# Optimization experiments

Hardware: AMD Instinct MI355X
Metric: run time of the kernel (lower is better)

Reference implementation:

```python
import jax, jax.numpy as jnp
import numpy as np

N = 20000      # nodes in both graphs
B = 128        # graphs in batch
E = 320000     # edges (avg degree 16)
F_IN = 768     # num_features (bert/graph feature dim)
RAW_F = 5000   # raw feature dim (hardcoded 5000 in source)
H = 256        # nhid
C = 4          # num_classes


def _gcn(x, src, dst, W, b):
    # PyG GCNConv: add self loops, symmetric D^-1/2 (A+I) D^-1/2 normalization
    n = x.shape[0]
    h = x @ W
    loop = jnp.arange(n, dtype=src.dtype)
    s = jnp.concatenate([src, loop])
    d = jnp.concatenate([dst, loop])
    deg = jax.ops.segment_sum(jnp.ones_like(d, dtype=h.dtype), d, num_segments=n)
    dinv = jax.lax.rsqrt(jnp.maximum(deg, 1.0))
    norm = (dinv[s] * dinv[d])[:, None]
    out = jax.ops.segment_sum(h[s] * norm, d, num_segments=n)
    return out + b


def _segment_mean(x, seg, num_segments):
    s = jax.ops.segment_sum(x, seg, num_segments=num_segments)
    cnt = jax.ops.segment_sum(jnp.ones((x.shape[0],), x.dtype), seg, num_segments=num_segments)
    return s / jnp.maximum(cnt, 1.0)[:, None]


def _prelu(x, a):
    return jnp.where(x >= 0, x, a * x)


def setup_inputs():
    key = jax.random.key(0)
    k = jax.random.split(key, 16)
    graph_x = jax.random.normal(k[0], (N, F_IN), jnp.float32)
    bert_x = jax.random.normal(k[1], (N, F_IN), jnp.float32)
    data_x = jax.random.normal(k[2], (N, RAW_F), jnp.float32) * 0.05
    edge_index = jax.random.randint(k[3], (2, E), 0, N, jnp.int32)
    raw_edge_index = jax.random.randint(k[4], (2, E), 0, N, jnp.int32)
    batch = ((jnp.arange(N) * B) // N).astype(jnp.int32)  # sorted, covers all B graphs
    rootindex = jax.random.randint(k[5], (B,), 0, N, jnp.int32)

    def lin(kk, fin, fout):
        return jax.random.normal(kk, (fin, fout), jnp.float32) * (1.0 / np.sqrt(fin))

    W1 = lin(k[6], F_IN, H); b1 = jnp.zeros((H,), jnp.float32)
    Wc0 = lin(k[7], RAW_F, H); bc0 = jnp.zeros((H,), jnp.float32)
    Wc1 = lin(k[8], H, H); bc1 = jnp.zeros((H,), jnp.float32)
    Wc2 = lin(k[9], H, H); bc2 = jnp.zeros((H,), jnp.float32)
    Wl1 = lin(k[10], 2 * RAW_F, 2 * H); bl1 = jnp.zeros((2 * H,), jnp.float32)
    Wl2 = lin(k[11], 2 * H, H); bl2 = jnp.zeros((H,), jnp.float32)
    W5 = lin(k[12], 5 * H, C); b5 = jnp.zeros((C,), jnp.float32)
    prelu_a = jnp.asarray(0.25, jnp.float32)
    return dict(graph_x=graph_x, bert_x=bert_x, data_x=data_x,
                edge_index=edge_index, raw_edge_index=raw_edge_index,
                graph_batch=batch, x_batch=batch, rootindex=rootindex,
                W1=W1, b1=b1, Wc0=Wc0, bc0=bc0, Wc1=Wc1, bc1=bc1, Wc2=Wc2, bc2=bc2,
                Wl1=Wl1, bl1=bl1, Wl2=Wl2, bl2=bl2, prelu_a=prelu_a, W5=W5, b5=b5)


def reference(graph_x, bert_x, data_x, edge_index, raw_edge_index, graph_batch,
              x_batch, rootindex, W1, b1, Wc0, bc0, Wc1, bc1, Wc2, bc2,
              Wl1, bl1, Wl2, bl2, prelu_a, W5, b5):
    # branch 1: GCNConv over graph_x (bert_user=0), relu, global max pool
    x = jax.nn.relu(_gcn(graph_x, edge_index[0], edge_index[1], W1, b1))
    x = jax.ops.segment_max(x, graph_batch, num_segments=B)   # [B, H]
    # branch 2: scatter_mean of raw features + root node, MLP w/ PReLU (eval: dropout = id)
    new_x = _segment_mean(data_x, x_batch, B)                 # [B, RAW_F]
    root = data_x[rootindex]                                  # [B, RAW_F]
    new_x = jnp.concatenate([new_x, root], axis=1)            # [B, 2*RAW_F]
    new_x = _prelu(new_x @ Wl1 + bl1, prelu_a)
    new_x = _prelu(new_x @ Wl2 + bl2, prelu_a)                # [B, H]
    # branch 3 (boost=1): 3 GCN layers over raw graph, mean pool each layer
    x_one = data_x
    pools = []
    for (W, b) in ((Wc0, bc0), (Wc1, bc1), (Wc2, bc2)):
        x_one = jax.nn.relu(_gcn(x_one, raw_edge_index[0], raw_edge_index[1], W, b))
        pools.append(_segment_mean(x_one, x_batch, B))
    out = jnp.concatenate(pools + [new_x, x], axis=1)         # [B, 5*H]
    return jax.nn.log_softmax(out @ W5 + b5, axis=1)
```

## Files before the change

kernel.cpp:

```cpp
#include <hip/hip_runtime.h>
#include <math.h>

#define NN   20000
#define BG   128
#define EE   320000
#define FIN  768
#define RAWF 5000
#define KP   5120
#define CATK 10240
#define HD   256
#define NC   4

typedef __attribute__((ext_vector_type(4))) float          f32x4;
typedef __attribute__((ext_vector_type(8))) unsigned short u16x8;
typedef __attribute__((ext_vector_type(4))) unsigned short u16x4;
typedef __attribute__((ext_vector_type(8))) __bf16         bf16x8;

__device__ __forceinline__ unsigned short f2bf(float f) {
  unsigned u = __float_as_uint(f);
  u += 0x7FFFu + ((u >> 16) & 1u);
  return (unsigned short)(u >> 16);
}
__device__ __forceinline__ float bf2f(unsigned short u) {
  return __uint_as_float((unsigned)u << 16);
}

static inline int ceil_div(int a, int b) { return (a + b - 1) / b; }

__global__ void count_deg2_k(const int* __restrict__ ei, const int* __restrict__ rei,
                             int* __restrict__ deg1, int* __restrict__ deg2) {
  int i = blockIdx.x * 256 + threadIdx.x;
  if (i < EE) atomicAdd(&deg1[ei[EE + i]], 1);
  else if (i < 2 * EE) atomicAdd(&deg2[rei[i]], 1);
}

__global__ __launch_bounds__(1024) void scan_local_k(const int* __restrict__ deg1,
                                                     const int* __restrict__ deg2,
                                                     int* __restrict__ excl,
                                                     int* __restrict__ bsum, int nb) {
  const int* deg = blockIdx.y ? deg2 : deg1;
  int* ex = excl + (size_t)blockIdx.y * NN;
  int* bs = bsum + (size_t)blockIdx.y * nb;
  __shared__ int wsum[16];
  int t = threadIdx.x, lane = t & 63, w = t >> 6;
  int i = blockIdx.x * 1024 + t;
  int v = (i < NN) ? deg[i] : 0;
  int acc = v;
#pragma unroll
  for (int off = 1; off < 64; off <<= 1) {
    int o = __shfl_up(acc, off, 64);
    if (lane >= off) acc += o;
  }
  if (lane == 63) wsum[w] = acc;
  __syncthreads();
  if (w == 0 && lane < 16) {
    int s = wsum[lane];
#pragma unroll
    for (int off = 1; off < 16; off <<= 1) {
      int o = __shfl_up(s, off, 64);
      if (lane >= off) s += o;
    }
    wsum[lane] = s;
  }
  __syncthreads();
  if (w > 0) acc += wsum[w - 1];
  if (i < NN) ex[i] = acc - v;
  if (t == 1023) bs[blockIdx.x] = acc;
}

__global__ void scan_tops_k(const int* __restrict__ bsum, int* __restrict__ boff,
                            int* __restrict__ end1, int* __restrict__ end2, int nb) {
  if (threadIdx.x == 0) {
    int run = 0;
    for (int b = 0; b < nb; ++b) { boff[b] = run; run += bsum[b]; }
    *end1 = run;
    run = 0;
    for (int b = 0; b < nb; ++b) { boff[nb + b] = run; run += bsum[nb + b]; }
    *end2 = run;
  }
}

__global__ __launch_bounds__(1024) void scan_add_k(
    const int* __restrict__ excl, const int* __restrict__ boff,
    const int* __restrict__ deg1, const int* __restrict__ deg2,
    int* __restrict__ rp1, int* __restrict__ rp2,
    int* __restrict__ cur1, int* __restrict__ cur2,
    float* __restrict__ dv1, float* __restrict__ dv2, int nb) {
  int y = blockIdx.y;
  const int* deg = y ? deg2 : deg1;
  int* rp = y ? rp2 : rp1;
  int* cur = y ? cur2 : cur1;
  float* dv = y ? dv2 : dv1;
  int i = blockIdx.x * 1024 + threadIdx.x;
  if (i < NN) {
    int v = excl[(size_t)y * NN + i] + boff[y * nb + blockIdx.x];
    rp[i] = v;
    cur[i] = v;
    dv[i] = rsqrtf((float)(deg[i] + 1));
  }
}

__global__ void scatter_k(const int* __restrict__ ei, const int* __restrict__ rei,
                          int* __restrict__ cur1, int* __restrict__ cur2,
                          int* __restrict__ col1, int* __restrict__ col2) {
  int i = blockIdx.x * 256 + threadIdx.x;
  int y = blockIdx.y;
  if (i < EE) {
    const int* e = y ? rei : ei;
    int* cur = y ? cur2 : cur1;
    int* col = y ? col2 : col1;
    int d = e[EE + i];
    int p = atomicAdd(&cur[d], 1);
    col[p] = e[i];
  }
}

__global__ void segbounds_k(const int* __restrict__ batch, int* __restrict__ s,
                            int* __restrict__ e, int n) {
  int i = blockIdx.x * 256 + threadIdx.x;
  if (i >= n) return;
  int b = batch[i];
  if (i == 0 || batch[i - 1] != b) s[b] = i;
  if (i == n - 1 || batch[i + 1] != b) e[b] = i + 1;
}

__global__ __launch_bounds__(256) void trans_k(
    const float* __restrict__ i0, unsigned short* __restrict__ o0,
    const float* __restrict__ i1, unsigned short* __restrict__ o1,
    const float* __restrict__ i2, unsigned short* __restrict__ o2,
    const float* __restrict__ i3, unsigned short* __restrict__ o3,
    const float* __restrict__ i4, unsigned short* __restrict__ o4) {
  __shared__ unsigned short tile[32][34];
  int b = blockIdx.x;
  const float* in; unsigned short* out;
  int K, N, Kout, tx, lid;
  if (b < 192)        { in=i0; out=o0; K=768;   N=256; Kout=768;   tx=24;  lid=b; }
  else if (b < 1472)  { in=i1; out=o1; K=5000;  N=256; Kout=5120;  tx=160; lid=b-192; }
  else if (b < 1536)  { in=i2; out=o2; K=256;   N=256; Kout=256;   tx=8;   lid=b-1472; }
  else if (b < 1600)  { in=i3; out=o3; K=256;   N=256; Kout=256;   tx=8;   lid=b-1536; }
  else                { in=i4; out=o4; K=10000; N=512; Kout=10240; tx=320; lid=b-1600; }
  int k0 = (lid % tx) * 32, n0 = (lid / tx) * 32;
  int txx = threadIdx.x & 31, tyy = threadIdx.x >> 5;
#pragma unroll
  for (int r = 0; r < 32; r += 8) {
    int k = k0 + tyy + r, n = n0 + txx;
    float v = (k < K) ? in[(size_t)k * N + n] : 0.f;
    tile[tyy + r][txx] = f2bf(v);
  }
  __syncthreads();
#pragma unroll
  for (int r = 0; r < 32; r += 8) {
    int n = n0 + tyy + r, k = k0 + txx;
    out[(size_t)n * Kout + k] = tile[txx][tyy + r];
  }
}

__global__ void conv_graphx_k(const float* __restrict__ in, unsigned short* __restrict__ out) {
  size_t i = (size_t)(blockIdx.x * 256 + threadIdx.x) * 8;
  f32x4 a = *(const f32x4*)(in + i);
  f32x4 b = *(const f32x4*)(in + i + 4);
  u16x8 o;
  o[0]=f2bf(a[0]); o[1]=f2bf(a[1]); o[2]=f2bf(a[2]); o[3]=f2bf(a[3]);
  o[4]=f2bf(b[0]); o[5]=f2bf(b[1]); o[6]=f2bf(b[2]); o[7]=f2bf(b[3]);
  *(u16x8*)(out + i) = o;
}

__global__ __launch_bounds__(256) void conv_pool_k(const float* __restrict__ x,
                                                   unsigned short* __restrict__ xb,
                                                   unsigned short* __restrict__ cat,
                                                   const int* __restrict__ segs,
                                                   const int* __restrict__ sege) {
  int g = blockIdx.x;
  int c = blockIdx.y * 256 + threadIdx.x;
  int s = segs[g], e = sege[g];
  bool vc = c < RAWF;
  float sum = 0.f;
  if (xb) {
    int i = s;
    for (; i + 2 <= e; i += 2) {
      float v0 = 0.f, v1 = 0.f;
      if (vc) { v0 = x[(size_t)i * RAWF + c]; v1 = x[(size_t)(i + 1) * RAWF + c]; }
      xb[(size_t)i * KP + c] = f2bf(v0);
      xb[(size_t)(i + 1) * KP + c] = f2bf(v1);
      sum += v0 + v1;
    }
    for (; i < e; ++i) {
      float v = 0.f;
      if (vc) v = x[(size_t)i * RAWF + c];
      xb[(size_t)i * KP + c] = f2bf(v);
      sum += v;
    }
  } else if (vc) {
    float a0 = 0, a1 = 0, a2 = 0, a3 = 0;
    int i = s;
    for (; i + 4 <= e; i += 4) {
      a0 += x[(size_t)(i + 0) * RAWF + c];
      a1 += x[(size_t)(i + 1) * RAWF + c];
      a2 += x[(size_t)(i + 2) * RAWF + c];
      a3 += x[(size_t)(i + 3) * RAWF + c];
    }
    for (; i < e; ++i) a0 += x[(size_t)i * RAWF + c];
    sum = (a0 + a1) + (a2 + a3);
  }
  if (vc) cat[(size_t)g * CATK + c] = f2bf(sum / (float)(e - s));
}

__global__ void root_cat_k(const float* __restrict__ data_x, const int* __restrict__ root,
                           unsigned short* __restrict__ cat) {
  int g = blockIdx.x;
  int c = blockIdx.y * 256 + threadIdx.x;
  if (c >= CATK - RAWF) return;
  unsigned short v = 0;
  if (c < RAWF) v = f2bf(data_x[(size_t)root[g] * RAWF + c]);
  cat[(size_t)g * CATK + RAWF + c] = v;
}

template <bool ABF16>
__global__ __launch_bounds__(256) void gemm_k(
    const void* __restrict__ Av, int Astride,
    const unsigned short* __restrict__ Bt, int Bstride,
    float* __restrict__ C, int M, int N, int Kreal, int kchunk, int atomic_out) {
  __shared__ unsigned short As[128 * 40];
  __shared__ unsigned short Bs[128 * 40];
  const int tid = threadIdx.x;
  const int lane = tid & 63, wave = tid >> 6;
  const int quad = lane >> 4, l16 = lane & 15;
  const int koff = quad * 8;
  const int bn = blockIdx.x * 128, bm = blockIdx.y * 128;
  const int wm = (wave >> 1) * 64, wn = (wave & 1) * 64;
  const int kbegin = blockIdx.z * kchunk;
  int kend = kbegin + kchunk; if (kend > Kreal) kend = Kreal;

  const int brow = tid >> 2, bcol = (tid & 3) * 8;
  const int arow_f = tid >> 3, acol_f = (tid & 7) * 4;

  u16x8 pb[2];
  u16x8 pa_b[2];
  f32x4 pa_f[4];

  auto load_tile = [&](int k0) {
#pragma unroll
    for (int i = 0; i < 2; ++i) {
      int gk = k0 + bcol;
      bool ok = ABF16 ? true : (gk + 8 <= kend);
      u16x8 v = (u16x8)(unsigned short)0;
      if (ok) v = *(const u16x8*)(Bt + (size_t)(bn + i * 64 + brow) * Bstride + gk);
      pb[i] = v;
    }
    if (ABF16) {
      const unsigned short* A = (const unsigned short*)Av;
#pragma unroll
      for (int i = 0; i < 2; ++i) {
        int r = bm + i * 64 + brow;
        u16x8 v = (u16x8)(unsigned short)0;
        if (r < M) v = *(const u16x8*)(A + (size_t)r * Astride + k0 + bcol);
        pa_b[i] = v;
      }
    } else {
      const float* A = (const float*)Av;
#pragma unroll
      for (int i = 0; i < 4; ++i) {
        int r = bm + i * 32 + arow_f;
        int gk = k0 + acol_f;
        f32x4 v = (f32x4)0.f;
        if (r < M && gk + 4 <= kend) v = *(const f32x4*)(A + (size_t)r * Astride + gk);
        pa_f[i] = v;
      }
    }
  };
  auto store_tile = [&]() {
#pragma unroll
    for (int i = 0; i < 2; ++i)
      *(u16x8*)&Bs[(i * 64 + brow) * 40 + bcol] = pb[i];
    if (ABF16) {
#pragma unroll
      for (int i = 0; i < 2; ++i)
        *(u16x8*)&As[(i * 64 + brow) * 40 + bcol] = pa_b[i];
    } else {
#pragma unroll
      for (int i = 0; i < 4; ++i) {
        u16x4 h;
        h[0] = f2bf(pa_f[i][0]); h[1] = f2bf(pa_f[i][1]);
        h[2] = f2bf(pa_f[i][2]); h[3] = f2bf(pa_f[i][3]);
        *(u16x4*)&As[(i * 32 + arow_f) * 40 + acol_f] = h;
      }
    }
  };

  f32x4 acc[4][4] = {};
  load_tile(kbegin);
  for (int k0 = kbegin; k0 < kend; k0 += 32) {
    store_tile();
    __syncthreads();
    int k1 = k0 + 32;
    if (k1 < kend) load_tile(k1);
    u16x8 ar[4], br[4];
#pragma unroll
    for (int i = 0; i < 4; ++i) ar[i] = *(const u16x8*)&As[(wm + i * 16 + l16) * 40 + koff];
#pragma unroll
    for (int j = 0; j < 4; ++j) br[j] = *(const u16x8*)&Bs[(wn + j * 16 + l16) * 40 + koff];
#pragma unroll
    for (int i = 0; i < 4; ++i)
#pragma unroll
      for (int j = 0; j < 4; ++j)
        acc[i][j] = __builtin_amdgcn_mfma_f32_16x16x32_bf16(
            __builtin_bit_cast(bf16x8, ar[i]), __builtin_bit_cast(bf16x8, br[j]),
            acc[i][j], 0, 0, 0);
    __syncthreads();
  }
#pragma unroll
  for (int i = 0; i < 4; ++i)
#pragma unroll
    for (int rr = 0; rr < 4; ++rr) {
      int grow = bm + wm + i * 16 + quad * 4 + rr;
      if (grow >= M) continue;
#pragma unroll
      for (int j = 0; j < 4; ++j) {
        int gcol = bn + wn + j * 16 + l16;
        if (gcol >= N) continue;
        float v = acc[i][j][rr];
        if (atomic_out) atomicAdd(&C[(size_t)grow * N + gcol], v);
        else C[(size_t)grow * N + gcol] = v;
      }
    }
}

__global__ __launch_bounds__(256) void gcn_agg_k(
    const float* __restrict__ h, const int* __restrict__ rowptr,
    const int* __restrict__ col, const float* __restrict__ dinv,
    const float* __restrict__ bias, unsigned short* __restrict__ outb, int n) {
  int wave = threadIdx.x >> 6, lane = threadIdx.x & 63;
  int node = blockIdx.x * 4 + wave;
  if (node >= n) return;
  int f = lane * 4;
  float di = dinv[node];
  f32x4 acc = *(const f32x4*)(h + (size_t)node * HD + f) * di;
  int beg = rowptr[node], end = rowptr[node + 1];
  int e = beg;
  for (; e + 4 <= end; e += 4) {
    int s0 = col[e], s1 = col[e + 1], s2 = col[e + 2], s3 = col[e + 3];
    float w0 = dinv[s0], w1 = dinv[s1], w2 = dinv[s2], w3 = dinv[s3];
    f32x4 h0 = *(const f32x4*)(h + (size_t)s0 * HD + f);
    f32x4 h1 = *(const f32x4*)(h + (size_t)s1 * HD + f);
    f32x4 h2 = *(const f32x4*)(h + (size_t)s2 * HD + f);
    f32x4 h3 = *(const f32x4*)(h + (size_t)s3 * HD + f);
    acc += h0 * w0; acc += h1 * w1; acc += h2 * w2; acc += h3 * w3;
  }
  for (; e < end; ++e) {
    int s = col[e];
    acc += *(const f32x4*)(h + (size_t)s * HD + f) * dinv[s];
  }
  f32x4 b = *(const f32x4*)(bias + f);
  acc = acc * di + b;
  u16x4 o;
#pragma unroll
  for (int q = 0; q < 4; ++q) o[q] = f2bf(fmaxf(acc[q], 0.f));
  *(u16x4*)(outb + (size_t)node * HD + f) = o;
}

__global__ __launch_bounds__(256) void seg_pool_bf16_k(const unsigned short* __restrict__ src,
                                                       const int* __restrict__ segs,
                                                       const int* __restrict__ sege,
                                                       float* __restrict__ dst, int dstride,
                                                       int doff, int mode) {
  int g = blockIdx.x, f = threadIdx.x;
  int s = segs[g], e = sege[g];
  float a0, a1, a2, a3;
  if (mode == 1) { a0 = a1 = a2 = a3 = -INFINITY; } else { a0 = a1 = a2 = a3 = 0.f; }
  int i = s;
  for (; i + 4 <= e; i += 4) {
    float v0 = bf2f(src[(size_t)(i + 0) * HD + f]);
    float v1 = bf2f(src[(size_t)(i + 1) * HD + f]);
    float v2 = bf2f(src[(size_t)(i + 2) * HD + f]);
    float v3 = bf2f(src[(size_t)(i + 3) * HD + f]);
    if (mode == 1) { a0 = fmaxf(a0, v0); a1 = fmaxf(a1, v1); a2 = fmaxf(a2, v2); a3 = fmaxf(a3, v3); }
    else           { a0 += v0; a1 += v1; a2 += v2; a3 += v3; }
  }
  for (; i < e; ++i) {
    float v = bf2f(src[(size_t)i * HD + f]);
    if (mode == 1) a0 = fmaxf(a0, v); else a0 += v;
  }
  float acc;
  if (mode == 1) acc = fmaxf(fmaxf(a0, a1), fmaxf(a2, a3));
  else {
    acc = (a0 + a1) + (a2 + a3);
    acc /= (float)((e - s) > 0 ? (e - s) : 1);
  }
  dst[(size_t)g * dstride + doff + f] = acc;
}

__global__ void bias_prelu_k(const float* __restrict__ in, const float* __restrict__ bias,
                             const float* __restrict__ pa, float* __restrict__ out,
                             int total, int cols) {
  int i = blockIdx.x * 256 + threadIdx.x;
  if (i >= total) return;
  float v = in[i] + bias[i % cols];
  float a = *pa;
  out[i] = (v >= 0.f) ? v : a * v;
}

__global__ __launch_bounds__(256) void gemm_e_k(const float* __restrict__ t1,
                                                const float* __restrict__ Wl2,
                                                const float* __restrict__ bl2,
                                                const float* __restrict__ pa,
                                                float* __restrict__ pools) {
  int b = blockIdx.x, n = threadIdx.x;
  float acc = 0.f;
  for (int k = 0; k < 512; ++k) acc = fmaf(t1[b * 512 + k], Wl2[k * 256 + n], acc);
  acc += bl2[n];
  float a = *pa;
  acc = (acc >= 0.f) ? acc : a * acc;
  pools[(size_t)b * 1280 + 768 + n] = acc;
}

__global__ __launch_bounds__(256) void final_k(const float* __restrict__ pools,
                                               const float* __restrict__ W5,
                                               const float* __restrict__ b5,
                                               float* __restrict__ out) {
  __shared__ float red[256][4];
  int b = blockIdx.x, t = threadIdx.x;
  float a0 = 0, a1 = 0, a2 = 0, a3 = 0;
  for (int i = t; i < 1280; i += 256) {
    float p = pools[(size_t)b * 1280 + i];
    a0 = fmaf(p, W5[i * 4 + 0], a0);
    a1 = fmaf(p, W5[i * 4 + 1], a1);
    a2 = fmaf(p, W5[i * 4 + 2], a2);
    a3 = fmaf(p, W5[i * 4 + 3], a3);
  }
  red[t][0] = a0; red[t][1] = a1; red[t][2] = a2; red[t][3] = a3;
  __syncthreads();
  for (int off = 128; off >= 1; off >>= 1) {
    if (t < off)
      for (int c = 0; c < 4; ++c) red[t][c] += red[t + off][c];
    __syncthreads();
  }
  if (t == 0) {
    float z[4];
    for (int c = 0; c < 4; ++c) z[c] = red[0][c] + b5[c];
    float m = fmaxf(fmaxf(z[0], z[1]), fmaxf(z[2], z[3]));
    float s = 0.f;
    for (int c = 0; c < 4; ++c) s += expf(z[c] - m);
    float lse = logf(s);
    for (int c = 0; c < 4; ++c) out[b * 4 + c] = z[c] - m - lse;
  }
}

extern "C" void kernel_launch(void* const* d_in, const int* in_sizes, int n_in,
                              void* d_out, int out_size, void* d_ws, size_t ws_size,
                              hipStream_t stream) {
  const float* graph_x = (const float*)d_in[0];
  const float* data_x  = (const float*)d_in[2];
  const int*   ei      = (const int*)d_in[3];
  const int*   rei     = (const int*)d_in[4];
  const int*   batch   = (const int*)d_in[5];
  const int*   rooti   = (const int*)d_in[7];
  const float* W1  = (const float*)d_in[8];   const float* b1  = (const float*)d_in[9];
  const float* Wc0 = (const float*)d_in[10];  const float* bc0 = (const float*)d_in[11];
  const float* Wc1 = (const float*)d_in[12];  const float* bc1 = (const float*)d_in[13];
  const float* Wc2 = (const float*)d_in[14];  const float* bc2 = (const float*)d_in[15];
  const float* Wl1 = (const float*)d_in[16];  const float* bl1 = (const float*)d_in[17];
  const float* Wl2 = (const float*)d_in[18];  const float* bl2 = (const float*)d_in[19];
  const float* pa  = (const float*)d_in[20];
  const float* W5  = (const float*)d_in[21];  const float* b5  = (const float*)d_in[22];
  float* out = (float*)d_out;

  char* ws = (char*)d_ws;
  size_t off = 0;
  auto take = [&](size_t bytes) -> void* {
    void* p = ws + off;
    off += (bytes + 255) & ~(size_t)255;
    return p;
  };
  const int NB = ceil_div(NN, 1024);

  int *deg1, *deg2, *rp1, *rp2, *cur1, *cur2, *col1, *col2, *excl, *bsum, *boff, *segs, *sege;
  float *dv1, *dv2, *hA, *Cd, *t1, *pools;
  unsigned short *W1t, *Wc0t, *Wc1t, *Wc2t, *Wl1t, *gxb, *catb, *hBb, *Axb;

  auto alloc_all = [&](bool withAxb) {
    off = 0;
    deg1 = (int*)take(NN * 4);   deg2 = (int*)take(NN * 4);
    rp1  = (int*)take((NN + 1) * 4); rp2 = (int*)take((NN + 1) * 4);
    cur1 = (int*)take(NN * 4);   cur2 = (int*)take(NN * 4);
    col1 = (int*)take(EE * 4);   col2 = (int*)take(EE * 4);
    dv1  = (float*)take(NN * 4); dv2  = (float*)take(NN * 4);
    excl = (int*)take((size_t)2 * NN * 4);
    bsum = (int*)take(2 * NB * 4); boff = (int*)take(2 * NB * 4);
    segs = (int*)take(BG * 4);   sege = (int*)take(BG * 4);
    W1t  = (unsigned short*)take((size_t)HD * FIN * 2);
    Wc0t = (unsigned short*)take((size_t)HD * KP * 2);
    Wc1t = (unsigned short*)take((size_t)HD * HD * 2);
    Wc2t = (unsigned short*)take((size_t)HD * HD * 2);
    Wl1t = (unsigned short*)take((size_t)512 * CATK * 2);
    gxb  = (unsigned short*)take((size_t)NN * FIN * 2);
    catb = (unsigned short*)take((size_t)BG * CATK * 2);
    Axb  = withAxb ? (unsigned short*)take((size_t)NN * KP * 2) : nullptr;
    hA   = (float*)take((size_t)NN * HD * 4);
    hBb  = (unsigned short*)take((size_t)NN * HD * 2);
    Cd   = (float*)take((size_t)BG * 512 * 4);
    t1   = (float*)take((size_t)BG * 512 * 4);
    pools = (float*)take((size_t)BG * 1280 * 4);
  };
  alloc_all(true);
  if (off > ws_size) alloc_all(false);
  const bool pathA = (Axb != nullptr);

  hipMemsetAsync(deg1, 0, (size_t)2 * ((NN * 4 + 255) & ~255), stream);
  hipMemsetAsync(Cd, 0, (size_t)BG * 512 * 4, stream);

  count_deg2_k<<<ceil_div(2 * EE, 256), 256, 0, stream>>>(ei, rei, deg1, deg2);
  scan_local_k<<<dim3(NB, 2), 1024, 0, stream>>>(deg1, deg2, excl, bsum, NB);
  scan_tops_k<<<1, 64, 0, stream>>>(bsum, boff, rp1 + NN, rp2 + NN, NB);
  scan_add_k<<<dim3(NB, 2), 1024, 0, stream>>>(excl, boff, deg1, deg2, rp1, rp2,
                                               cur1, cur2, dv1, dv2, NB);
  scatter_k<<<dim3(ceil_div(EE, 256), 2), 256, 0, stream>>>(ei, rei, cur1, cur2, col1, col2);
  segbounds_k<<<ceil_div(NN, 256), 256, 0, stream>>>(batch, segs, sege, NN);

  trans_k<<<6720, 256, 0, stream>>>(W1, W1t, Wc0, Wc0t, Wc1, Wc1t, Wc2, Wc2t, Wl1, Wl1t);

  conv_graphx_k<<<(NN * FIN) / (256 * 8), 256, 0, stream>>>(graph_x, gxb);
  conv_pool_k<<<dim3(BG, KP / 256), 256, 0, stream>>>(data_x, Axb, catb, segs, sege);
  root_cat_k<<<dim3(BG, ceil_div(CATK - RAWF, 256)), 256, 0, stream>>>(data_x, rooti, catb);

  int mt = ceil_div(NN, 128);

  hipMemsetAsync(hA, 0, (size_t)NN * HD * 4, stream);
  gemm_k<true><<<dim3(2, mt, 3), 256, 0, stream>>>(gxb, FIN, W1t, FIN, hA, NN, HD, FIN, 256, 1);
  gcn_agg_k<<<ceil_div(NN, 4), 256, 0, stream>>>(hA, rp1, col1, dv1, b1, hBb, NN);
  seg_pool_bf16_k<<<BG, 256, 0, stream>>>(hBb, segs, sege, pools, 1280, 1024, 1);

  hipMemsetAsync(hA, 0, (size_t)NN * HD * 4, stream);
  if (pathA)
    gemm_k<true><<<dim3(2, mt, 4), 256, 0, stream>>>(Axb, KP, Wc0t, KP, hA, NN, HD, KP, 1280, 1);
  else
    gemm_k<false><<<dim3(2, mt, 4), 256, 0, stream>>>(data_x, RAWF, Wc0t, KP, hA, NN, HD, RAWF, 1256, 1);
  gcn_agg_k<<<ceil_div(NN, 4), 256, 0, stream>>>(hA, rp2, col2, dv2, bc0, hBb, NN);
  seg_pool_bf16_k<<<BG, 256, 0, stream>>>(hBb, segs, sege, pools, 1280, 0, 0);

  hipMemsetAsync(hA, 0, (size_t)NN * HD * 4, stream);
  gemm_k<true><<<dim3(2, mt, 2), 256, 0, stream>>>(hBb, HD, Wc1t, HD, hA, NN, HD, HD, 128, 1);
  gcn_agg_k<<<ceil_div(NN, 4), 256, 0, stream>>>(hA, rp2, col2, dv2, bc1, hBb, NN);
  seg_pool_bf16_k<<<BG, 256, 0, stream>>>(hBb, segs, sege, pools, 1280, 256, 0);

  hipMemsetAsync(hA, 0, (size_t)NN * HD * 4, stream);
  gemm_k<true><<<dim3(2, mt, 2), 256, 0, stream>>>(hBb, HD, Wc2t, HD, hA, NN, HD, HD, 128, 1);
  gcn_agg_k<<<ceil_div(NN, 4), 256, 0, stream>>>(hA, rp2, col2, dv2, bc2, hBb, NN);
  seg_pool_bf16_k<<<BG, 256, 0, stream>>>(hBb, segs, sege, pools, 1280, 512, 0);

  gemm_k<true><<<dim3(4, 1, 32), 256, 0, stream>>>(catb, CATK, Wl1t, CATK, Cd, BG, 512, CATK, 320, 1);
  bias_prelu_k<<<ceil_div(BG * 512, 256), 256, 0, stream>>>(Cd, bl1, pa, t1, BG * 512, 512);
  gemm_e_k<<<BG, 256, 0, stream>>>(t1, Wl2, bl2, pa, pools);

  final_k<<<BG, 256, 0, stream>>>(pools, W5, b5, out);
}
```

Measured before the change: 1.369 ms.

## Fuse conversions, prescale GEMM rows by dinv, swizzle tiles, parallelize scan tops

Several independent changes land together. The graph_x bf16 conversion pass is removed so the first GEMM reads fp32 directly, and root gathering is merged into the vectorised pooling kernel. The source-side dinv is applied in the GEMM epilogue so the aggregation only sums neighbour rows, and bias+PReLU is folded into the second MLP kernel. It also adds a grouped tile remap for the 2-column GEMMs, changes split-K factors, and replaces the serial top-level scan with a warp scan. Together these drop launches and intermediate buffers, at the cost of fp32 A-tile loads in the first GEMM and less split-K parallelism.

```diff
diff --git a/kernel.cpp b/kernel.cpp
--- a/kernel.cpp
+++ b/kernel.cpp
@@ -70,13 +70,18 @@
 
 __global__ void scan_tops_k(const int* __restrict__ bsum, int* __restrict__ boff,
                             int* __restrict__ end1, int* __restrict__ end2, int nb) {
-  if (threadIdx.x == 0) {
-    int run = 0;
-    for (int b = 0; b < nb; ++b) { boff[b] = run; run += bsum[b]; }
-    *end1 = run;
-    run = 0;
-    for (int b = 0; b < nb; ++b) { boff[nb + b] = run; run += bsum[nb + b]; }
-    *end2 = run;
+  int t = threadIdx.x;
+  int half = t >> 5, idx = t & 31;
+  int v = (idx < nb) ? bsum[half * nb + idx] : 0;
+  int acc = v;
+#pragma unroll
+  for (int off = 1; off < 32; off <<= 1) {
+    int o = __shfl_up(acc, off, 32);
+    if (idx >= off) acc += o;
+  }
+  if (idx < nb) boff[half * nb + idx] = acc - v;
+  if (idx == nb - 1) {
+    if (half == 0) *end1 = acc; else *end2 = acc;
   }
 }
 
@@ -155,78 +160,75 @@
   }
 }
 
-__global__ void conv_graphx_k(const float* __restrict__ in, unsigned short* __restrict__ out) {
-  size_t i = (size_t)(blockIdx.x * 256 + threadIdx.x) * 8;
-  f32x4 a = *(const f32x4*)(in + i);
-  f32x4 b = *(const f32x4*)(in + i + 4);
-  u16x8 o;
-  o[0]=f2bf(a[0]); o[1]=f2bf(a[1]); o[2]=f2bf(a[2]); o[3]=f2bf(a[3]);
-  o[4]=f2bf(b[0]); o[5]=f2bf(b[1]); o[6]=f2bf(b[2]); o[7]=f2bf(b[3]);
-  *(u16x8*)(out + i) = o;
-}
-
 __global__ __launch_bounds__(256) void conv_pool_k(const float* __restrict__ x,
                                                    unsigned short* __restrict__ xb,
                                                    unsigned short* __restrict__ cat,
                                                    const int* __restrict__ segs,
-                                                   const int* __restrict__ sege) {
+                                                   const int* __restrict__ sege,
+                                                   const int* __restrict__ root) {
   int g = blockIdx.x;
-  int c = blockIdx.y * 256 + threadIdx.x;
+  if (blockIdx.y >= KP / 256) {
+    int c = (blockIdx.y - KP / 256) * 256 + threadIdx.x;
+    if (c < CATK - RAWF) {
+      unsigned short v = 0;
+      if (c < RAWF) v = f2bf(x[(size_t)root[g] * RAWF + c]);
+      cat[(size_t)g * CATK + RAWF + c] = v;
+    }
+    return;
+  }
+  __shared__ f32x4 part[4][64];
+  int wave = threadIdx.x >> 6, lane = threadIdx.x & 63;
+  int c = blockIdx.y * 256 + lane * 4;
   int s = segs[g], e = sege[g];
-  bool vc = c < RAWF;
-  float sum = 0.f;
-  if (xb) {
-    int i = s;
-    for (; i + 2 <= e; i += 2) {
-      float v0 = 0.f, v1 = 0.f;
-      if (vc) { v0 = x[(size_t)i * RAWF + c]; v1 = x[(size_t)(i + 1) * RAWF + c]; }
-      xb[(size_t)i * KP + c] = f2bf(v0);
-      xb[(size_t)(i + 1) * KP + c] = f2bf(v1);
-      sum += v0 + v1;
-    }
-    for (; i < e; ++i) {
-      float v = 0.f;
-      if (vc) v = x[(size_t)i * RAWF + c];
-      xb[(size_t)i * KP + c] = f2bf(v);
-      sum += v;
-    }
-  } else if (vc) {
-    float a0 = 0, a1 = 0, a2 = 0, a3 = 0;
-    int i = s;
-    for (; i + 4 <= e; i += 4) {
-      a0 += x[(size_t)(i + 0) * RAWF + c];
-      a1 += x[(size_t)(i + 1) * RAWF + c];
-      a2 += x[(size_t)(i + 2) * RAWF + c];
-      a3 += x[(size_t)(i + 3) * RAWF + c];
-    }
-    for (; i < e; ++i) a0 += x[(size_t)i * RAWF + c];
-    sum = (a0 + a1) + (a2 + a3);
-  }
-  if (vc) cat[(size_t)g * CATK + c] = f2bf(sum / (float)(e - s));
-}
-
-__global__ void root_cat_k(const float* __restrict__ data_x, const int* __restrict__ root,
-                           unsigned short* __restrict__ cat) {
-  int g = blockIdx.x;
-  int c = blockIdx.y * 256 + threadIdx.x;
-  if (c >= CATK - RAWF) return;
-  unsigned short v = 0;
-  if (c < RAWF) v = f2bf(data_x[(size_t)root[g] * RAWF + c]);
-  cat[(size_t)g * CATK + RAWF + c] = v;
+  bool v4 = (c + 4 <= RAWF);
+  f32x4 sum = (f32x4)0.f;
+  for (int i = s + wave; i < e; i += 4) {
+    f32x4 v = (f32x4)0.f;
+    if (v4) v = *(const f32x4*)(x + (size_t)i * RAWF + c);
+    if (xb) {
+      u16x4 h;
+      h[0] = f2bf(v[0]); h[1] = f2bf(v[1]); h[2] = f2bf(v[2]); h[3] = f2bf(v[3]);
+      *(u16x4*)(xb + (size_t)i * KP + c) = h;
+    }
+    sum += v;
+  }
+  part[wave][lane] = sum;
+  __syncthreads();
+  if (threadIdx.x < 64 && v4) {
+    f32x4 tot = part[0][lane] + part[1][lane] + part[2][lane] + part[3][lane];
+    float cnt = (float)(e - s);
+    u16x4 o;
+    o[0] = f2bf(tot[0] / cnt); o[1] = f2bf(tot[1] / cnt);
+    o[2] = f2bf(tot[2] / cnt); o[3] = f2bf(tot[3] / cnt);
+    *(u16x4*)(cat + (size_t)g * CATK + c) = o;
+  }
 }
 
 template <bool ABF16>
 __global__ __launch_bounds__(256) void gemm_k(
     const void* __restrict__ Av, int Astride,
     const unsigned short* __restrict__ Bt, int Bstride,
-    float* __restrict__ C, int M, int N, int Kreal, int kchunk, int atomic_out) {
+    float* __restrict__ C, const float* __restrict__ escale,
+    int M, int N, int Kreal, int kchunk, int atomic_out) {
   __shared__ unsigned short As[128 * 40];
   __shared__ unsigned short Bs[128 * 40];
   const int tid = threadIdx.x;
   const int lane = tid & 63, wave = tid >> 6;
   const int quad = lane >> 4, l16 = lane & 15;
   const int koff = quad * 8;
-  const int bn = blockIdx.x * 128, bm = blockIdx.y * 128;
+
+  int xt = blockIdx.x, yt = blockIdx.y;
+  if (gridDim.x == 2) {
+    const int MT = gridDim.y;
+    int flat = (yt << 1) | xt;
+    int gp = flat >> 4;
+    int ybase = gp << 3;
+    int rem = MT - ybase;
+    int j = flat & 15;
+    if (rem >= 8) { xt = j >> 3; yt = ybase + (j & 7); }
+    else          { xt = (j >= rem); yt = ybase + (xt ? j - rem : j); }
+  }
+  const int bn = xt * 128, bm = yt * 128;
   const int wm = (wave >> 1) * 64, wn = (wave & 1) * 64;
   const int kbegin = blockIdx.z * kchunk;
   int kend = kbegin + kchunk; if (kend > Kreal) kend = Kreal;
@@ -314,11 +316,12 @@
     for (int rr = 0; rr < 4; ++rr) {
       int grow = bm + wm + i * 16 + quad * 4 + rr;
       if (grow >= M) continue;
+      float sc = escale ? escale[grow] : 1.f;
 #pragma unroll
       for (int j = 0; j < 4; ++j) {
         int gcol = bn + wn + j * 16 + l16;
         if (gcol >= N) continue;
-        float v = acc[i][j][rr];
+        float v = acc[i][j][rr] * sc;
         if (atomic_out) atomicAdd(&C[(size_t)grow * N + gcol], v);
         else C[(size_t)grow * N + gcol] = v;
       }
@@ -333,23 +336,20 @@
   int node = blockIdx.x * 4 + wave;
   if (node >= n) return;
   int f = lane * 4;
-  float di = dinv[node];
-  f32x4 acc = *(const f32x4*)(h + (size_t)node * HD + f) * di;
+  f32x4 acc = *(const f32x4*)(h + (size_t)node * HD + f);
   int beg = rowptr[node], end = rowptr[node + 1];
   int e = beg;
   for (; e + 4 <= end; e += 4) {
     int s0 = col[e], s1 = col[e + 1], s2 = col[e + 2], s3 = col[e + 3];
-    float w0 = dinv[s0], w1 = dinv[s1], w2 = dinv[s2], w3 = dinv[s3];
     f32x4 h0 = *(const f32x4*)(h + (size_t)s0 * HD + f);
     f32x4 h1 = *(const f32x4*)(h + (size_t)s1 * HD + f);
     f32x4 h2 = *(const f32x4*)(h + (size_t)s2 * HD + f);
     f32x4 h3 = *(const f32x4*)(h + (size_t)s3 * HD + f);
-    acc += h0 * w0; acc += h1 * w1; acc += h2 * w2; acc += h3 * w3;
-  }
-  for (; e < end; ++e) {
-    int s = col[e];
-    acc += *(const f32x4*)(h + (size_t)s * HD + f) * dinv[s];
-  }
+    acc += h0; acc += h1; acc += h2; acc += h3;
+  }
+  for (; e < end; ++e)
+    acc += *(const f32x4*)(h + (size_t)col[e] * HD + f);
+  float di = dinv[node];
   f32x4 b = *(const f32x4*)(bias + f);
   acc = acc * di + b;
   u16x4 o;
@@ -389,26 +389,23 @@
   dst[(size_t)g * dstride + doff + f] = acc;
 }
 
-__global__ void bias_prelu_k(const float* __restrict__ in, const float* __restrict__ bias,
-                             const float* __restrict__ pa, float* __restrict__ out,
-                             int total, int cols) {
-  int i = blockIdx.x * 256 + threadIdx.x;
-  if (i >= total) return;
-  float v = in[i] + bias[i % cols];
-  float a = *pa;
-  out[i] = (v >= 0.f) ? v : a * v;
-}
-
-__global__ __launch_bounds__(256) void gemm_e_k(const float* __restrict__ t1,
+__global__ __launch_bounds__(256) void gemm_e_k(const float* __restrict__ Cd,
+                                                const float* __restrict__ bl1,
                                                 const float* __restrict__ Wl2,
                                                 const float* __restrict__ bl2,
                                                 const float* __restrict__ pa,
                                                 float* __restrict__ pools) {
+  __shared__ float t[512];
   int b = blockIdx.x, n = threadIdx.x;
+  float a = *pa;
+  for (int k = n; k < 512; k += 256) {
+    float v = Cd[(size_t)b * 512 + k] + bl1[k];
+    t[k] = (v >= 0.f) ? v : a * v;
+  }
+  __syncthreads();
   float acc = 0.f;
-  for (int k = 0; k < 512; ++k) acc = fmaf(t1[b * 512 + k], Wl2[k * 256 + n], acc);
+  for (int k = 0; k < 512; ++k) acc = fmaf(t[k], Wl2[k * 256 + n], acc);
   acc += bl2[n];
-  float a = *pa;
   acc = (acc >= 0.f) ? acc : a * acc;
   pools[(size_t)b * 1280 + 768 + n] = acc;
 }
@@ -474,8 +471,8 @@
   const int NB = ceil_div(NN, 1024);
 
   int *deg1, *deg2, *rp1, *rp2, *cur1, *cur2, *col1, *col2, *excl, *bsum, *boff, *segs, *sege;
-  float *dv1, *dv2, *hA, *Cd, *t1, *pools;
-  unsigned short *W1t, *Wc0t, *Wc1t, *Wc2t, *Wl1t, *gxb, *catb, *hBb, *Axb;
+  float *dv1, *dv2, *hA, *Cd, *pools;
+  unsigned short *W1t, *Wc0t, *Wc1t, *Wc2t, *Wl1t, *catb, *hBb, *Axb;
 
   auto alloc_all = [&](bool withAxb) {
     off = 0;
@@ -492,13 +489,11 @@
     Wc1t = (unsigned short*)take((size_t)HD * HD * 2);
     Wc2t = (unsigned short*)take((size_t)HD * HD * 2);
     Wl1t = (unsigned short*)take((size_t)512 * CATK * 2);
-    gxb  = (unsigned short*)take((size_t)NN * FIN * 2);
     catb = (unsigned short*)take((size_t)BG * CATK * 2);
     Axb  = withAxb ? (unsigned short*)take((size_t)NN * KP * 2) : nullptr;
     hA   = (float*)take((size_t)NN * HD * 4);
     hBb  = (unsigned short*)take((size_t)NN * HD * 2);
     Cd   = (float*)take((size_t)BG * 512 * 4);
-    t1   = (float*)take((size_t)BG * 512 * 4);
     pools = (float*)take((size_t)BG * 1280 * 4);
   };
   alloc_all(true);
@@ -518,38 +513,42 @@
 
   trans_k<<<6720, 256, 0, stream>>>(W1, W1t, Wc0, Wc0t, Wc1, Wc1t, Wc2, Wc2t, Wl1, Wl1t);
 
-  conv_graphx_k<<<(NN * FIN) / (256 * 8), 256, 0, stream>>>(graph_x, gxb);
-  conv_pool_k<<<dim3(BG, KP / 256), 256, 0, stream>>>(data_x, Axb, catb, segs, sege);
-  root_cat_k<<<dim3(BG, ceil_div(CATK - RAWF, 256)), 256, 0, stream>>>(data_x, rooti, catb);
+  conv_pool_k<<<dim3(BG, KP / 256 + ceil_div(CATK - RAWF, 256)), 256, 0, stream>>>(
+      data_x, Axb, catb, segs, sege, rooti);
 
   int mt = ceil_div(NN, 128);
 
   hipMemsetAsync(hA, 0, (size_t)NN * HD * 4, stream);
-  gemm_k<true><<<dim3(2, mt, 3), 256, 0, stream>>>(gxb, FIN, W1t, FIN, hA, NN, HD, FIN, 256, 1);
+  gemm_k<false><<<dim3(2, mt, 2), 256, 0, stream>>>(graph_x, FIN, W1t, FIN, hA, dv1,
+                                                    NN, HD, FIN, 384, 1);
   gcn_agg_k<<<ceil_div(NN, 4), 256, 0, stream>>>(hA, rp1, col1, dv1, b1, hBb, NN);
   seg_pool_bf16_k<<<BG, 256, 0, stream>>>(hBb, segs, sege, pools, 1280, 1024, 1);
 
   hipMemsetAsync(hA, 0, (size_t)NN * HD * 4, stream);
   if (pathA)
-    gemm_k<true><<<dim3(2, mt, 4), 256, 0, stream>>>(Axb, KP, Wc0t, KP, hA, NN, HD, KP, 1280, 1);
+    gemm_k<true><<<dim3(2, mt, 2), 256, 0, stream>>>(Axb, KP, Wc0t, KP, hA, dv2,
+                                                     NN, HD, KP, 2560, 1);
   else
-    gemm_k<false><<<dim3(2, mt, 4), 256, 0, stream>>>(data_x, RAWF, Wc0t, KP, hA, NN, HD, RAWF, 1256, 1);
+    gemm_k<false><<<dim3(2, mt, 4), 256, 0, stream>>>(data_x, RAWF, Wc0t, KP, hA, dv2,
+                                                      NN, HD, RAWF, 1256, 1);
   gcn_agg_k<<<ceil_div(NN, 4), 256, 0, stream>>>(hA, rp2, col2, dv2, bc0, hBb, NN);
   seg_pool_bf16_k<<<BG, 256, 0, stream>>>(hBb, segs, sege, pools, 1280, 0, 0);
 
   hipMemsetAsync(hA, 0, (size_t)NN * HD * 4, stream);
-  gemm_k<true><<<dim3(2, mt, 2), 256, 0, stream>>>(hBb, HD, Wc1t, HD, hA, NN, HD, HD, 128, 1);
+  gemm_k<true><<<dim3(2, mt, 2), 256, 0, stream>>>(hBb, HD, Wc1t, HD, hA, dv2,
+                                                   NN, HD, HD, 128, 1);
   gcn_agg_k<<<ceil_div(NN, 4), 256, 0, stream>>>(hA, rp2, col2, dv2, bc1, hBb, NN);
   seg_pool_bf16_k<<<BG, 256, 0, stream>>>(hBb, segs, sege, pools, 1280, 256, 0);
 
   hipMemsetAsync(hA, 0, (size_t)NN * HD * 4, stream);
-  gemm_k<true><<<dim3(2, mt, 2), 256, 0, stream>>>(hBb, HD, Wc2t, HD, hA, NN, HD, HD, 128, 1);
+  gemm_k<true><<<dim3(2, mt, 2), 256, 0, stream>>>(hBb, HD, Wc2t, HD, hA, dv2,
+                                                   NN, HD, HD, 128, 1);
   gcn_agg_k<<<ceil_div(NN, 4), 256, 0, stream>>>(hA, rp2, col2, dv2, bc2, hBb, NN);
   seg_pool_bf16_k<<<BG, 256, 0, stream>>>(hBb, segs, sege, pools, 1280, 512, 0);
 
-  gemm_k<true><<<dim3(4, 1, 32), 256, 0, stream>>>(catb, CATK, Wl1t, CATK, Cd, BG, 512, CATK, 320, 1);
-  bias_prelu_k<<<ceil_div(BG * 512, 256), 256, 0, stream>>>(Cd, bl1, pa, t1, BG * 512, 512);
-  gemm_e_k<<<BG, 256, 0, stream>>>(t1, Wl2, bl2, pa, pools);
+  gemm_k<true><<<dim3(4, 1, 32), 256, 0, stream>>>(catb, CATK, Wl1t, CATK, Cd, nullptr,
+                                                   BG, 512, CATK, 320, 1);
+  gemm_e_k<<<BG, 256, 0, stream>>>(Cd, bl1, Wl2, bl2, pa, pools);
 
   final_k<<<BG, 256, 0, stream>>>(pools, W5, b5, out);
 }
```

Result: no change. 1.356 ms (-0.9%).
